# Kernel tuning notes

Hardware: AMD Instinct MI355X
Metric: run time of the kernel (lower is better)

The kernel has to match this reference:

```python
import jax, jax.numpy as jnp
import numpy as np

N, D, E, F, TOP_K = 4096, 1024, 8, 2048, 2


def setup_inputs() -> dict:
    key = jax.random.key(0)
    ks = jax.random.split(key, 4)
    x = jax.random.normal(ks[0], (N, D), jnp.float32)
    # MoE-style routing: dense scores, keep top-2 per token, zeros elsewhere
    scores = jax.random.uniform(ks[1], (N, E), jnp.float32)
    topv, _ = jax.lax.top_k(scores, TOP_K)
    routing_tensor = jnp.where(scores >= topv[:, -1:], scores, 0.0)
    # expert weights init: uniform(-1/sqrt(fan_out), 1/sqrt(fan_out)) per BatchedExperts.init_
    s0 = 1.0 / np.sqrt(F).astype(np.float32)
    s1 = 1.0 / np.sqrt(D).astype(np.float32)
    w0 = jax.random.uniform(ks[2], (E, D, F), jnp.float32, -s0, s0)
    b0 = jnp.zeros((E, 1, F), jnp.float32)
    w1 = jax.random.uniform(ks[3], (E, F, D), jnp.float32, -s1, s1)
    b1 = jnp.zeros((E, 1, D), jnp.float32)
    return {"x": x, "routing_tensor": routing_tensor, "w0": w0, "b0": b0, "w1": w1, "b1": b1}


def reference(x, routing_tensor, w0, b0, w1, b1):
    # depth=2, bias=True. Each expert: act(x @ W0 + b0) @ W1 + b1, scaled by its
    # routing score and summed over experts. Tokens with score 0 contribute 0,
    # identical math to the original's mask-gather / scatter-add dispatch.
    h = jax.nn.gelu(jnp.einsum('nd,edf->enf', x, w0) + b0, approximate=False)  # [E,N,F]
    y = jnp.einsum('enf,efd->end', h, w1) + b1                                  # [E,N,D]
    return jnp.einsum('ne,end->nd', routing_tensor, y)                          # [N,D]
```

## Files before the change

kernel.cpp:

```cpp
#include <hip/hip_runtime.h>

#define N_TOK 4096
#define DIM   1024
#define NEXP  8
#define FDIM  2048
#define CAP   2048

typedef __attribute__((ext_vector_type(8))) short short8;
typedef __attribute__((ext_vector_type(4))) float f32x4;

__device__ __forceinline__ unsigned short f2bf(float f) {
  union { float f; unsigned u; } v; v.f = f;
  unsigned r = v.u + 0x7fffu + ((v.u >> 16) & 1u);
  return (unsigned short)(r >> 16);
}

__device__ __forceinline__ void async_cp16(const void* g, void* l) {
  __builtin_amdgcn_global_load_lds((const __attribute__((address_space(1))) unsigned int*)g,
                                   (__attribute__((address_space(3))) unsigned int*)l,
                                   16, 0, 0);
}

__global__ void zero_counts_k(int* counts) {
  if (threadIdx.x < NEXP) counts[threadIdx.x] = 0;
}

__global__ void transpose_conv_k(const float* __restrict__ in, unsigned short* __restrict__ out,
                                 int R, int C) {
  __shared__ float tile[32][33];
  int tpc = C / 32, tpr = R / 32;
  int b = blockIdx.x;
  int e = b / (tpr * tpc);
  int rem = b % (tpr * tpc);
  int rt = rem / tpc, ct = rem % tpc;
  const float* inp = in + (size_t)e * R * C;
  unsigned short* outp = out + (size_t)e * R * C;
  int tx = threadIdx.x & 31, ty = threadIdx.x >> 5;
  int r0 = rt * 32, c0 = ct * 32;
#pragma unroll
  for (int i = 0; i < 4; i++)
    tile[ty + 8 * i][tx] = inp[(size_t)(r0 + ty + 8 * i) * C + c0 + tx];
  __syncthreads();
#pragma unroll
  for (int i = 0; i < 4; i++)
    outp[(size_t)(c0 + ty + 8 * i) * R + r0 + tx] = f2bf(tile[tx][ty + 8 * i]);
}

__global__ void build_lists_k(const float* __restrict__ routing, int* counts,
                              int* idx, float* wgt) {
  int n = blockIdx.x * blockDim.x + threadIdx.x;
  if (n >= N_TOK) return;
  for (int e = 0; e < NEXP; e++) {
    float s = routing[(size_t)n * NEXP + e];
    if (s > 0.0f) {
      int pos = atomicAdd(&counts[e], 1);
      if (pos < CAP) { idx[e * CAP + pos] = n; wgt[e * CAP + pos] = s; }
    }
  }
}

__global__ void gather_pad_k(const float* __restrict__ x, const int* __restrict__ counts,
                             int* __restrict__ idx, float* __restrict__ wgt,
                             unsigned short* __restrict__ Xg) {
  int b = blockIdx.x;
  int e = b / CAP, i = b % CAP;
  int cnt = counts[e];
  int cntR = min((cnt + 127) & ~127, CAP);
  if (i >= cntR) return;
  int t = threadIdx.x;
  unsigned short* row = Xg + (size_t)(e * CAP + i) * DIM;
  if (i < cnt) {
    int n = idx[e * CAP + i];
    const float4* xr = (const float4*)(x + (size_t)n * DIM);
    float4 v = xr[t];
    ushort4 o;
    o.x = f2bf(v.x); o.y = f2bf(v.y); o.z = f2bf(v.z); o.w = f2bf(v.w);
    ((ushort4*)row)[t] = o;
  } else {
    ((ushort4*)row)[t] = make_ushort4(0, 0, 0, 0);
    if (t == 0) { idx[e * CAP + i] = 0; wgt[e * CAP + i] = 0.0f; }
  }
}

template <int EPI, int KDIM, int NCOLS>
__global__ __launch_bounds__(256, 2) void gemm_k(
    const unsigned short* __restrict__ A, const unsigned short* __restrict__ Bt,
    const float* __restrict__ bias, const int* __restrict__ counts,
    const int* __restrict__ idx, const float* __restrict__ wgt,
    unsigned short* __restrict__ Hout, float* __restrict__ out) {
  __shared__ unsigned short lsA[128 * 64];
  __shared__ unsigned short lsB[128 * 64];
  constexpr int MT = CAP / 128;
  constexpr int NT = NCOLS / 128;
  int b = blockIdx.x;
  int e = b / (MT * NT);
  int rem = b % (MT * NT);
  int mt = rem / NT, nt = rem % NT;
  int cnt = counts[e];
  int cntR = min((cnt + 127) & ~127, CAP);
  int m0 = mt * 128;
  if (m0 >= cntR) return;
  int n0 = nt * 128;

  const unsigned short* Ae = A + (size_t)e * CAP * KDIM;
  const unsigned short* Be = Bt + (size_t)e * NCOLS * KDIM;

  int tid = threadIdx.x;
  int lane = tid & 63;
  int w = tid >> 6;
  int wr = w >> 1, wc = w & 1;

  f32x4 acc[4][4];
#pragma unroll
  for (int m = 0; m < 4; m++)
#pragma unroll
    for (int n = 0; n < 4; n++) acc[m][n] = (f32x4){0.f, 0.f, 0.f, 0.f};

  int srow = lane >> 3;
  int scl = (lane & 7) ^ srow;
  for (int k0 = 0; k0 < KDIM; k0 += 64) {
#pragma unroll
    for (int j = 0; j < 4; j++) {
      int ch = w * 4 + j;
      int row = ch * 8 + srow;
      async_cp16(Ae + (size_t)(m0 + row) * KDIM + k0 + scl * 8, &lsA[ch * 512]);
      async_cp16(Be + (size_t)(n0 + row) * KDIM + k0 + scl * 8, &lsB[ch * 512]);
    }
    __syncthreads();
#pragma unroll
    for (int ks = 0; ks < 2; ks++) {
      short8 av[4], bv[4];
#pragma unroll
      for (int m = 0; m < 4; m++) {
        int r = wr * 64 + m * 16 + (lane & 15);
        int cp = (ks * 4 + (lane >> 4)) ^ (r & 7);
        av[m] = *(const short8*)&lsA[r * 64 + cp * 8];
      }
#pragma unroll
      for (int n = 0; n < 4; n++) {
        int r = wc * 64 + n * 16 + (lane & 15);
        int cp = (ks * 4 + (lane >> 4)) ^ (r & 7);
        bv[n] = *(const short8*)&lsB[r * 64 + cp * 8];
      }
#pragma unroll
      for (int m = 0; m < 4; m++)
#pragma unroll
        for (int n = 0; n < 4; n++)
          acc[m][n] = __builtin_amdgcn_mfma_f32_16x16x32_bf16(av[m], bv[n], acc[m][n], 0, 0, 0);
    }
    __syncthreads();
  }

  int lr = (lane >> 4) * 4;
  int lc = lane & 15;
#pragma unroll
  for (int n = 0; n < 4; n++) {
    int gc = n0 + wc * 64 + n * 16 + lc;
    float bb = bias[e * NCOLS + gc];
#pragma unroll
    for (int m = 0; m < 4; m++) {
      int gr = m0 + wr * 64 + m * 16 + lr;
      f32x4 v = acc[m][n];
#pragma unroll
      for (int r = 0; r < 4; r++) {
        int row = gr + r;
        float t = v[r] + bb;
        if (EPI == 0) {
          float g = t * 0.5f * (1.0f + erff(t * 0.70710678118f));
          Hout[(size_t)(e * CAP + row) * NCOLS + gc] = f2bf(g);
        } else {
          int token = idx[e * CAP + row];
          float wv = wgt[e * CAP + row];
          atomicAdd(out + (size_t)token * NCOLS + gc, t * wv);
        }
      }
    }
  }
}

extern "C" void kernel_launch(void* const* d_in, const int* in_sizes, int n_in,
                              void* d_out, int out_size, void* d_ws, size_t ws_size,
                              hipStream_t stream) {
  const float* x  = (const float*)d_in[0];
  const float* rt = (const float*)d_in[1];
  const float* w0 = (const float*)d_in[2];
  const float* b0 = (const float*)d_in[3];
  const float* w1 = (const float*)d_in[4];
  const float* b1 = (const float*)d_in[5];
  float* out = (float*)d_out;

  char* ws = (char*)d_ws;
  int* counts = (int*)ws;
  int* idx    = (int*)(ws + 256);
  float* wgt  = (float*)(ws + 256 + 65536);
  unsigned short* w0T = (unsigned short*)(ws + 256 + 2 * 65536);
  unsigned short* w1T = w0T + (size_t)NEXP * DIM * FDIM;
  unsigned short* Xg  = w1T + (size_t)NEXP * DIM * FDIM;
  unsigned short* Hb  = Xg + (size_t)NEXP * CAP * DIM;

  hipMemsetAsync(d_out, 0, (size_t)N_TOK * DIM * sizeof(float), stream);
  zero_counts_k<<<1, 64, 0, stream>>>(counts);
  transpose_conv_k<<<NEXP * (DIM / 32) * (FDIM / 32), 256, 0, stream>>>(w0, w0T, DIM, FDIM);
  transpose_conv_k<<<NEXP * (FDIM / 32) * (DIM / 32), 256, 0, stream>>>(w1, w1T, FDIM, DIM);
  build_lists_k<<<N_TOK / 256, 256, 0, stream>>>(rt, counts, idx, wgt);
  gather_pad_k<<<NEXP * CAP, 256, 0, stream>>>(x, counts, idx, wgt, Xg);
  gemm_k<0, DIM, FDIM><<<NEXP * (CAP / 128) * (FDIM / 128), 256, 0, stream>>>(
      Xg, w0T, b0, counts, idx, wgt, Hb, nullptr);
  gemm_k<1, FDIM, DIM><<<NEXP * (CAP / 128) * (DIM / 128), 256, 0, stream>>>(
      Hb, w1T, b1, counts, idx, wgt, nullptr, out);
}
```

Before: 378.5 us.

## Triple-buffer GEMM LDS pipeline with 256x128 tiles and 8-wave blocks

Rewrites the expert GEMM main loop so global-to-LDS async copies are issued two K-steps ahead into a three-slot ring, using a partial vmcnt wait and a barrier instead of two full syncthreads per step. The tile grows to 256x128 with 512 threads, padding moves to multiples of 256, and block indices are remapped to interleave experts across the grid. It also raises MFMA wave priority during compute. The aim is to hide load latency behind matrix math, at the cost of more LDS (about 144KB per block), which limits occupancy, and extra padded rows.

After: 504.1 us. 1.33x slower.

```diff
diff --git a/kernel.cpp b/kernel.cpp
--- a/kernel.cpp
+++ b/kernel.cpp
@@ -65,7 +65,7 @@
   int b = blockIdx.x;
   int e = b / CAP, i = b % CAP;
   int cnt = counts[e];
-  int cntR = min((cnt + 127) & ~127, CAP);
+  int cntR = min((cnt + 255) & ~255, CAP);
   if (i >= cntR) return;
   int t = threadIdx.x;
   unsigned short* row = Xg + (size_t)(e * CAP + i) * DIM;
@@ -83,24 +83,29 @@
 }
 
 template <int EPI, int KDIM, int NCOLS>
-__global__ __launch_bounds__(256, 2) void gemm_k(
+__global__ __launch_bounds__(512, 2) void gemm_k(
     const unsigned short* __restrict__ A, const unsigned short* __restrict__ Bt,
     const float* __restrict__ bias, const int* __restrict__ counts,
     const int* __restrict__ idx, const float* __restrict__ wgt,
     unsigned short* __restrict__ Hout, float* __restrict__ out) {
-  __shared__ unsigned short lsA[128 * 64];
-  __shared__ unsigned short lsB[128 * 64];
-  constexpr int MT = CAP / 128;
-  constexpr int NT = NCOLS / 128;
+  constexpr int BM = 256, BN = 128, BK = 64;
+  constexpr int KT = KDIM / BK;
+  constexpr int MT = CAP / BM;
+  constexpr int NT = NCOLS / BN;
+  constexpr int BUFE = BM * BK + BN * BK;
+  __shared__ unsigned short lds[3 * BUFE];
+
+  int nwg = NEXP * MT * NT;
   int b = blockIdx.x;
+  b = (b & 7) * (nwg >> 3) + (b >> 3);
   int e = b / (MT * NT);
   int rem = b % (MT * NT);
   int mt = rem / NT, nt = rem % NT;
   int cnt = counts[e];
-  int cntR = min((cnt + 127) & ~127, CAP);
-  int m0 = mt * 128;
+  int cntR = min((cnt + 255) & ~255, CAP);
+  int m0 = mt * BM;
   if (m0 >= cntR) return;
-  int n0 = nt * 128;
+  int n0 = nt * BN;
 
   const unsigned short* Ae = A + (size_t)e * CAP * KDIM;
   const unsigned short* Be = Bt + (size_t)e * NCOLS * KDIM;
@@ -108,25 +113,43 @@
   int tid = threadIdx.x;
   int lane = tid & 63;
   int w = tid >> 6;
-  int wr = w >> 1, wc = w & 1;
-
-  f32x4 acc[4][4];
-#pragma unroll
-  for (int m = 0; m < 4; m++)
-#pragma unroll
-    for (int n = 0; n < 4; n++) acc[m][n] = (f32x4){0.f, 0.f, 0.f, 0.f};
+  int wr = w & 3, wc = w >> 2;
 
   int srow = lane >> 3;
   int scl = (lane & 7) ^ srow;
-  for (int k0 = 0; k0 < KDIM; k0 += 64) {
-#pragma unroll
-    for (int j = 0; j < 4; j++) {
-      int ch = w * 4 + j;
-      int row = ch * 8 + srow;
-      async_cp16(Ae + (size_t)(m0 + row) * KDIM + k0 + scl * 8, &lsA[ch * 512]);
-      async_cp16(Be + (size_t)(n0 + row) * KDIM + k0 + scl * 8, &lsB[ch * 512]);
-    }
-    __syncthreads();
+
+  auto stage = [&](int buf, int k0) {
+    unsigned short* bp = &lds[buf * BUFE];
+#pragma unroll
+    for (int r = 0; r < 4; r++) {
+      int ch = r * 8 + w;
+      async_cp16(Ae + (size_t)(m0 + ch * 8 + srow) * KDIM + k0 + scl * 8, bp + ch * 512);
+    }
+#pragma unroll
+    for (int r = 0; r < 2; r++) {
+      int ch = r * 8 + w;
+      async_cp16(Be + (size_t)(n0 + ch * 8 + srow) * KDIM + k0 + scl * 8,
+                 bp + BM * BK + ch * 512);
+    }
+  };
+
+  f32x4 acc[4][4];
+#pragma unroll
+  for (int m = 0; m < 4; m++)
+#pragma unroll
+    for (int n = 0; n < 4; n++) acc[m][n] = (f32x4){0.f, 0.f, 0.f, 0.f};
+
+  stage(0, 0);
+  stage(1, BK);
+  asm volatile("s_waitcnt vmcnt(6)\n\ts_barrier" ::: "memory");
+
+  int ibc = 0, ibs = 2;
+#pragma unroll 1
+  for (int t = 0; t < KT; ++t) {
+    if (t + 2 < KT) stage(ibs, (t + 2) * BK);
+    const unsigned short* bp = &lds[ibc * BUFE];
+    const unsigned short* bpB = bp + BM * BK;
+    __builtin_amdgcn_s_setprio(1);
 #pragma unroll
     for (int ks = 0; ks < 2; ks++) {
       short8 av[4], bv[4];
@@ -134,13 +157,13 @@
       for (int m = 0; m < 4; m++) {
         int r = wr * 64 + m * 16 + (lane & 15);
         int cp = (ks * 4 + (lane >> 4)) ^ (r & 7);
-        av[m] = *(const short8*)&lsA[r * 64 + cp * 8];
+        av[m] = *(const short8*)&bp[r * 64 + cp * 8];
       }
 #pragma unroll
       for (int n = 0; n < 4; n++) {
         int r = wc * 64 + n * 16 + (lane & 15);
         int cp = (ks * 4 + (lane >> 4)) ^ (r & 7);
-        bv[n] = *(const short8*)&lsB[r * 64 + cp * 8];
+        bv[n] = *(const short8*)&bpB[r * 64 + cp * 8];
       }
 #pragma unroll
       for (int m = 0; m < 4; m++)
@@ -148,7 +171,13 @@
         for (int n = 0; n < 4; n++)
           acc[m][n] = __builtin_amdgcn_mfma_f32_16x16x32_bf16(av[m], bv[n], acc[m][n], 0, 0, 0);
     }
-    __syncthreads();
+    __builtin_amdgcn_s_setprio(0);
+    if (t + 1 < KT) {
+      if (t + 2 < KT) asm volatile("s_waitcnt vmcnt(6)\n\ts_barrier" ::: "memory");
+      else            asm volatile("s_waitcnt vmcnt(0)\n\ts_barrier" ::: "memory");
+    }
+    ibc = (ibc == 2) ? 0 : ibc + 1;
+    ibs = (ibs == 2) ? 0 : ibs + 1;
   }
 
   int lr = (lane >> 4) * 4;
@@ -164,14 +193,14 @@
 #pragma unroll
       for (int r = 0; r < 4; r++) {
         int row = gr + r;
-        float t = v[r] + bb;
+        float tv = v[r] + bb;
         if (EPI == 0) {
-          float g = t * 0.5f * (1.0f + erff(t * 0.70710678118f));
+          float g = tv * 0.5f * (1.0f + erff(tv * 0.70710678118f));
           Hout[(size_t)(e * CAP + row) * NCOLS + gc] = f2bf(g);
         } else {
           int token = idx[e * CAP + row];
           float wv = wgt[e * CAP + row];
-          atomicAdd(out + (size_t)token * NCOLS + gc, t * wv);
+          atomicAdd(out + (size_t)token * NCOLS + gc, tv * wv);
         }
       }
     }
@@ -204,8 +233,8 @@
   transpose_conv_k<<<NEXP * (FDIM / 32) * (DIM / 32), 256, 0, stream>>>(w1, w1T, FDIM, DIM);
   build_lists_k<<<N_TOK / 256, 256, 0, stream>>>(rt, counts, idx, wgt);
   gather_pad_k<<<NEXP * CAP, 256, 0, stream>>>(x, counts, idx, wgt, Xg);
-  gemm_k<0, DIM, FDIM><<<NEXP * (CAP / 128) * (FDIM / 128), 256, 0, stream>>>(
+  gemm_k<0, DIM, FDIM><<<NEXP * (CAP / 256) * (FDIM / 128), 512, 0, stream>>>(
       Xg, w0T, b0, counts, idx, wgt, Hb, nullptr);
-  gemm_k<1, FDIM, DIM><<<NEXP * (CAP / 128) * (DIM / 128), 256, 0, stream>>>(
+  gemm_k<1, FDIM, DIM><<<NEXP * (CAP / 256) * (DIM / 128), 512, 0, stream>>>(
       Hb, w1T, b1, counts, idx, wgt, nullptr, out);
 }
```
